# Kernel optimization log

Measured on AMD Instinct MI355X. Metric: run time of the kernel, lower is better.

The kernel has to match this reference:

```python
import jax, jax.numpy as jnp
import numpy as np


def _lstm_layer(x, Wx, Wh, b):
    """Standard LSTM over time. x: [B,T,D], Wx/Wh: [D,4D], b: [4D]. Returns [B,T,D]."""
    B, T, D = x.shape
    # Precompute input contributions for all timesteps (one big GEMM).
    xg = jnp.einsum('btd,dg->btg', x, Wx) + b  # [B,T,4D]

    def step(carry, xg_t):
        h, c = carry
        g = xg_t + h @ Wh  # [B,4D]
        i, f, gg, o = jnp.split(g, 4, axis=-1)
        c = jax.nn.sigmoid(f) * c + jax.nn.sigmoid(i) * jnp.tanh(gg)
        h = jax.nn.sigmoid(o) * jnp.tanh(c)
        return (h, c), h

    h0 = jnp.zeros((B, D), x.dtype)
    c0 = jnp.zeros((B, D), x.dtype)
    (_, _), hs = jax.lax.scan(step, (h0, c0), jnp.swapaxes(xg, 0, 1))  # hs: [T,B,D]
    return jnp.swapaxes(hs, 0, 1)


def setup_inputs() -> dict:
    key = jax.random.key(0)
    ks = jax.random.split(key, 8)
    B, T, V, D = 4, 1024, 32000, 512
    s = 1.0 / np.sqrt(D)
    return {
        'tokens': jax.random.randint(ks[0], (B, T), 0, V, dtype=jnp.int32),
        'embed': jax.random.normal(ks[1], (V, D), jnp.float32),  # stddev=1.0 per embedding_init
        'Wx0': jax.random.normal(ks[2], (D, 4 * D), jnp.float32) * s,
        'Wh0': jax.random.normal(ks[3], (D, 4 * D), jnp.float32) * s,
        'b0': jnp.zeros((4 * D,), jnp.float32),
        'Wx1': jax.random.normal(ks[4], (D, 4 * D), jnp.float32) * s,
        'Wh1': jax.random.normal(ks[5], (D, 4 * D), jnp.float32) * s,
        'b1': jnp.zeros((4 * D,), jnp.float32),
        'Wout': jax.random.normal(ks[6], (D, V), jnp.float32) * s,
        'bout': jnp.zeros((V,), jnp.float32),
    }


def reference(tokens, embed, Wx0, Wh0, b0, Wx1, Wh1, b1, Wout, bout):
    # ShiftRight(axis=1): prepend 0 token, drop last.
    shifted = jnp.pad(tokens, ((0, 0), (1, 0)))[:, :-1]
    x = jnp.take(embed, shifted, axis=0)  # [B,T,D]
    x = _lstm_layer(x, Wx0, Wh0, b0)
    x = _lstm_layer(x, Wx1, Wh1, b1)
    # Dropout is deterministic=True -> identity.
    logits = jnp.einsum('btd,dv->btv', x, Wout) + bout  # [B,T,V]
    return logits
```

## Files before the change

kernel.cpp:

```cpp
#include <hip/hip_runtime.h>
#include <math.h>


#define TSEQ 1024
#define DIM  512
#define GDIM 2048
#define VOC  32000
#define SENT 0x7F7F7F7Fu

typedef unsigned uint4v __attribute__((ext_vector_type(4)));
typedef float    f4v    __attribute__((ext_vector_type(4)));
typedef short    short8 __attribute__((ext_vector_type(8)));
typedef float    f32x4  __attribute__((ext_vector_type(4)));

__device__ __forceinline__ uint4v poll_load16(const unsigned* p) {
    uint4v v;
    asm volatile("global_load_dwordx4 %0, %1, off sc1\n\t"
                 "s_waitcnt vmcnt(0)"
                 : "=v"(v) : "v"(p) : "memory");
    return v;
}

__device__ __forceinline__ float fsig(float x) {
    return __builtin_amdgcn_rcpf(1.0f + __expf(-x));
}
__device__ __forceinline__ float ftanh_(float x) {
    return 1.0f - 2.0f * __builtin_amdgcn_rcpf(1.0f + __expf(2.0f * x));
}

__device__ __forceinline__ unsigned short f2bf(float x) {
    unsigned u = __builtin_bit_cast(unsigned, x);
    return (unsigned short)((u + 0x7FFFu + ((u >> 16) & 1u)) >> 16);
}
__device__ __forceinline__ float bf2f(unsigned short h) {
    return __builtin_bit_cast(float, (unsigned)h << 16);
}

__global__ void embed_kernel(const int* __restrict__ tokens,
                             const float* __restrict__ embed,
                             float* __restrict__ x)
{
    const int row = blockIdx.x;
    const int b = row >> 10;
    const int t = row & 1023;
    const int tok = (t == 0) ? 0 : tokens[b * TSEQ + t - 1];
    const float4* src = (const float4*)(embed + (size_t)tok * DIM);
    float4* dst = (float4*)(x + (size_t)row * DIM);
    dst[threadIdx.x] = src[threadIdx.x];
}

__global__ __launch_bounds__(256) void gemm_bias_f32(
    const float* __restrict__ A, const float* __restrict__ Bm,
    const float* __restrict__ bias, float* __restrict__ C,
    int M, int N, int K)
{
    constexpr int BK = 16;
    __shared__ float As[BK][128 + 4];
    __shared__ float Bs[BK][128 + 4];

    const int tid = threadIdx.x;
    const int m0 = blockIdx.y * 128;
    const int n0 = blockIdx.x * 128;
    const int tm = (tid >> 4) << 3;
    const int tn = (tid & 15) << 3;

    const int a_r = tid >> 2;
    const int a_c = (tid & 3) << 2;
    const int b_r = tid >> 5;
    const int b_c = (tid & 31) << 2;

    float acc[8][8] = {};

    for (int k0 = 0; k0 < K; k0 += BK) {
        const float4 av0 = *(const float4*)&A[(size_t)(m0 + a_r) * K + k0 + a_c];
        const float4 av1 = *(const float4*)&A[(size_t)(m0 + a_r + 64) * K + k0 + a_c];
        const float4 bv0 = *(const float4*)&Bm[(size_t)(k0 + b_r) * N + n0 + b_c];
        const float4 bv1 = *(const float4*)&Bm[(size_t)(k0 + b_r + 8) * N + n0 + b_c];
        __syncthreads();
        As[a_c + 0][a_r] = av0.x;  As[a_c + 1][a_r] = av0.y;
        As[a_c + 2][a_r] = av0.z;  As[a_c + 3][a_r] = av0.w;
        As[a_c + 0][a_r + 64] = av1.x;  As[a_c + 1][a_r + 64] = av1.y;
        As[a_c + 2][a_r + 64] = av1.z;  As[a_c + 3][a_r + 64] = av1.w;
        *(float4*)&Bs[b_r][b_c] = bv0;
        *(float4*)&Bs[b_r + 8][b_c] = bv1;
        __syncthreads();

        #pragma unroll
        for (int kk = 0; kk < BK; ++kk) {
            float a[8], bf[8];
            *(float4*)&a[0]  = *(const float4*)&As[kk][tm];
            *(float4*)&a[4]  = *(const float4*)&As[kk][tm + 4];
            *(float4*)&bf[0] = *(const float4*)&Bs[kk][tn];
            *(float4*)&bf[4] = *(const float4*)&Bs[kk][tn + 4];
            #pragma unroll
            for (int i = 0; i < 8; ++i)
                #pragma unroll
                for (int jx = 0; jx < 8; ++jx)
                    acc[i][jx] += a[i] * bf[jx];
        }
    }

    float bv[8];
    #pragma unroll
    for (int jx = 0; jx < 8; ++jx) bv[jx] = bias[n0 + tn + jx];

    #pragma unroll
    for (int i = 0; i < 8; ++i) {
        float* crow = C + (size_t)(m0 + tm + i) * N + (n0 + tn);
        float4 o0, o1;
        o0.x = acc[i][0] + bv[0]; o0.y = acc[i][1] + bv[1];
        o0.z = acc[i][2] + bv[2]; o0.w = acc[i][3] + bv[3];
        o1.x = acc[i][4] + bv[4]; o1.y = acc[i][5] + bv[5];
        o1.z = acc[i][6] + bv[6]; o1.w = acc[i][7] + bv[7];
        *(float4*)&crow[0] = o0;
        *(float4*)&crow[4] = o1;
    }
}

__global__ __launch_bounds__(512, 1) void lstm2_kernel(
    const float* __restrict__ xg1, const float* __restrict__ Wh0,
    const float* __restrict__ Wx1, const float* __restrict__ Wh1,
    const float* __restrict__ b1,
    float* __restrict__ h1c, float* __restrict__ h2c,
    float* __restrict__ hs2)
{
    const int layer = blockIdx.x >> 6;
    const int wg    = blockIdx.x & 63;
    const int tid   = threadIdx.x;
    const int dbase = wg * 8;
    const int j = tid & 31;
    const int s = tid >> 5;
    const int wcol = (j >> 3) * DIM + dbase + (j & 7);

    __shared__ f4v  hA[DIM];
    __shared__ f4v  hB[DIM];
    __shared__ float part[16][4][32];
    __shared__ float gate_lds[4][32];

    float wr[32], wx[32];
    {
        const float* Wrec = layer ? Wh1 : Wh0;
        #pragma unroll
        for (int r = 0; r < 32; ++r)
            wr[r] = Wrec[(size_t)(s * 32 + r) * GDIM + wcol];
        if (layer) {
            #pragma unroll
            for (int r = 0; r < 32; ++r)
                wx[r] = Wx1[(size_t)(s * 32 + r) * GDIM + wcol];
        }
    }
    float bias2 = 0.f;
    if (layer && tid < 128) bias2 = b1[wcol];

    float c_reg = 0.f;
    const unsigned* h1u = (const unsigned*)h1c;
    const unsigned* h2u = (const unsigned*)h2c;

    if (layer == 0) {
        for (int t = 0; t < TSEQ; ++t) {
            float xgv = 0.f;
            if (tid < 128) xgv = xg1[((size_t)s * TSEQ + t) * GDIM + wcol];

            if (t > 0) {
                const unsigned* p = h1u + ((size_t)(t - 1) * DIM + tid) * 4;
                uint4v u;
                do { u = poll_load16(p); }
                while (u.x == SENT || u.y == SENT || u.z == SENT || u.w == SENT);
                hA[tid] = __builtin_bit_cast(f4v, u);
            } else {
                hA[tid] = f4v{0.f, 0.f, 0.f, 0.f};
            }
            __syncthreads();

            float a0 = 0.f, a1 = 0.f, a2 = 0.f, a3 = 0.f;
            const f4v* hp = &hA[s * 32];
            #pragma unroll
            for (int r = 0; r < 32; ++r) {
                const f4v v = hp[r];
                a0 += v.x * wr[r]; a1 += v.y * wr[r];
                a2 += v.z * wr[r]; a3 += v.w * wr[r];
            }
            part[s][0][j] = a0; part[s][1][j] = a1;
            part[s][2][j] = a2; part[s][3][j] = a3;
            __syncthreads();

            if (tid < 128) {
                float sum = xgv;
                #pragma unroll
                for (int s2 = 0; s2 < 16; ++s2) sum += part[s2][s][j];
                gate_lds[s][j] = sum;
            }
            __syncthreads();

            if (tid < 32) {
                const int ub = tid >> 3, ud = tid & 7;
                const float iv = gate_lds[ub][ 0 + ud];
                const float fv = gate_lds[ub][ 8 + ud];
                const float gv = gate_lds[ub][16 + ud];
                const float ov = gate_lds[ub][24 + ud];
                const float ig = fsig(iv);
                const float fg = fsig(fv);
                const float og = fsig(ov);
                c_reg = fg * c_reg + ig * ftanh_(gv);
                const float hval = og * ftanh_(c_reg);
                __hip_atomic_store(&h1c[((size_t)t * DIM + dbase + ud) * 4 + ub],
                                   hval, __ATOMIC_RELAXED, __HIP_MEMORY_SCOPE_AGENT);
            }
        }
    } else {
        for (int t = 0; t < TSEQ; ++t) {
            if (t > 0) {
                const unsigned* p = h2u + ((size_t)(t - 1) * DIM + tid) * 4;
                uint4v u;
                do { u = poll_load16(p); }
                while (u.x == SENT || u.y == SENT || u.z == SENT || u.w == SENT);
                hB[tid] = __builtin_bit_cast(f4v, u);
            } else {
                hB[tid] = f4v{0.f, 0.f, 0.f, 0.f};
            }
            __syncthreads();

            float a0 = 0.f, a1 = 0.f, a2 = 0.f, a3 = 0.f;
            {
                const f4v* hp = &hB[s * 32];
                #pragma unroll
                for (int r = 0; r < 32; ++r) {
                    const f4v v = hp[r];
                    a0 += v.x * wr[r]; a1 += v.y * wr[r];
                    a2 += v.z * wr[r]; a3 += v.w * wr[r];
                }
            }

            {
                const unsigned* p = h1u + ((size_t)t * DIM + tid) * 4;
                uint4v u;
                do { u = poll_load16(p); }
                while (u.x == SENT || u.y == SENT || u.z == SENT || u.w == SENT);
                hA[tid] = __builtin_bit_cast(f4v, u);
            }
            __syncthreads();
            {
                const f4v* hp = &hA[s * 32];
                #pragma unroll
                for (int r = 0; r < 32; ++r) {
                    const f4v v = hp[r];
                    a0 += v.x * wx[r]; a1 += v.y * wx[r];
                    a2 += v.z * wx[r]; a3 += v.w * wx[r];
                }
            }
            part[s][0][j] = a0; part[s][1][j] = a1;
            part[s][2][j] = a2; part[s][3][j] = a3;
            __syncthreads();

            if (tid < 128) {
                float sum = bias2;
                #pragma unroll
                for (int s2 = 0; s2 < 16; ++s2) sum += part[s2][s][j];
                gate_lds[s][j] = sum;
            }
            __syncthreads();

            if (tid < 32) {
                const int ub = tid >> 3, ud = tid & 7;
                const float iv = gate_lds[ub][ 0 + ud];
                const float fv = gate_lds[ub][ 8 + ud];
                const float gv = gate_lds[ub][16 + ud];
                const float ov = gate_lds[ub][24 + ud];
                const float ig = fsig(iv);
                const float fg = fsig(fv);
                const float og = fsig(ov);
                c_reg = fg * c_reg + ig * ftanh_(gv);
                const float hval = og * ftanh_(c_reg);
                __hip_atomic_store(&h2c[((size_t)t * DIM + dbase + ud) * 4 + ub],
                                   hval, __ATOMIC_RELAXED, __HIP_MEMORY_SCOPE_AGENT);
                hs2[((size_t)ub * TSEQ + t) * DIM + dbase + ud] = hval;
            }
        }
    }
}

__global__ __launch_bounds__(256) void transpose_W(const float* __restrict__ W,
                                                   unsigned short* __restrict__ Wt)
{
    __shared__ float tile[32][256];
    const int tid = threadIdx.x;
    const int n0 = blockIdx.x * 256;
    const int k0 = blockIdx.y * 32;

    #pragma unroll 8
    for (int r = 0; r < 32; ++r)
        tile[r][tid] = W[(size_t)(k0 + r) * VOC + n0 + tid];
    __syncthreads();

    unsigned short pr[64];
    #pragma unroll
    for (int kk = 0; kk < 32; ++kk) {
        const float w = tile[kk][tid];
        const unsigned short h = f2bf(w);
        const unsigned short l = f2bf(w - bf2f(h));
        pr[2 * kk + 0] = h;
        pr[2 * kk + 1] = l;
    }
    unsigned short* dst = Wt + (size_t)(n0 + tid) * 1024 + 2 * k0;
    #pragma unroll
    for (int i = 0; i < 8; ++i)
        *(short8*)(dst + 8 * i) = *(short8*)&pr[8 * i];
}

__global__ __launch_bounds__(64) void convert_A(const float* __restrict__ A,
                                                unsigned short* __restrict__ At)
{
    const int row = blockIdx.x;
    const int tid = threadIdx.x;
    const float4 v0 = *(const float4*)&A[(size_t)row * DIM + tid * 8];
    const float4 v1 = *(const float4*)&A[(size_t)row * DIM + tid * 8 + 4];
    float vals[8] = {v0.x, v0.y, v0.z, v0.w, v1.x, v1.y, v1.z, v1.w};
    unsigned short pr[16];
    #pragma unroll
    for (int i = 0; i < 8; ++i) {
        const unsigned short h = f2bf(vals[i]);
        pr[2 * i + 0] = h;
        pr[2 * i + 1] = h;
    }
    unsigned short* dst = At + (size_t)row * 1024 + tid * 16;
    #pragma unroll
    for (int i = 0; i < 2; ++i)
        *(short8*)(dst + 8 * i) = *(short8*)&pr[8 * i];
}

__global__ __launch_bounds__(256) void mfma_logits(
    const unsigned short* __restrict__ Ab, const unsigned short* __restrict__ Wb,
    const float* __restrict__ bias, float* __restrict__ C)
{
    constexpr int KP = 1024, BK = 64, NKT = KP / BK;
    __shared__ unsigned short As[128 * 64];
    __shared__ unsigned short Bs[128 * 64];

    const int tid  = threadIdx.x;
    const int lane = tid & 63;
    const int w    = tid >> 6;
    const int wm   = w >> 1, wn = w & 1;
    const int m0 = blockIdx.y * 128;
    const int n0 = blockIdx.x * 128;

    const int srow = tid >> 1;
    const int s0   = (tid & 1) * 4;
    const unsigned short* gA = Ab + (size_t)(m0 + srow) * KP + s0 * 8;
    const unsigned short* gB = Wb + (size_t)(n0 + srow) * KP + s0 * 8;
    const int swz = srow & 7;

    f32x4 acc[4][4] = {};
    short8 ra[4], rb[4];

    #pragma unroll
    for (int c = 0; c < 4; ++c) {
        ra[c] = *(const short8*)(gA + c * 8);
        rb[c] = *(const short8*)(gB + c * 8);
    }

    #pragma unroll 1
    for (int kt = 0; kt < NKT; ++kt) {
        __syncthreads();
        #pragma unroll
        for (int c = 0; c < 4; ++c) {
            *(short8*)&As[srow * 64 + ((s0 + c) ^ swz) * 8] = ra[c];
            *(short8*)&Bs[srow * 64 + ((s0 + c) ^ swz) * 8] = rb[c];
        }
        __syncthreads();

        if (kt + 1 < NKT) {
            const int ko = (kt + 1) * BK;
            #pragma unroll
            for (int c = 0; c < 4; ++c) {
                ra[c] = *(const short8*)(gA + ko + c * 8);
                rb[c] = *(const short8*)(gB + ko + c * 8);
            }
        }

        #pragma unroll
        for (int kk = 0; kk < 2; ++kk) {
            const int q = kk * 4 + (lane >> 4);
            short8 a[4], b[4];
            #pragma unroll
            for (int i = 0; i < 4; ++i) {
                const int Ra = wm * 64 + i * 16 + (lane & 15);
                a[i] = *(const short8*)&As[Ra * 64 + (q ^ (Ra & 7)) * 8];
                const int Rb = wn * 64 + i * 16 + (lane & 15);
                b[i] = *(const short8*)&Bs[Rb * 64 + (q ^ (Rb & 7)) * 8];
            }
            #pragma unroll
            for (int i = 0; i < 4; ++i)
                #pragma unroll
                for (int jx = 0; jx < 4; ++jx)
                    acc[i][jx] = __builtin_amdgcn_mfma_f32_16x16x32_bf16(
                        a[i], b[jx], acc[i][jx], 0, 0, 0);
        }
    }

    float bv[4];
    #pragma unroll
    for (int jx = 0; jx < 4; ++jx)
        bv[jx] = bias[n0 + wn * 64 + jx * 16 + (lane & 15)];

    #pragma unroll
    for (int i = 0; i < 4; ++i) {
        #pragma unroll
        for (int jx = 0; jx < 4; ++jx) {
            const int col = n0 + wn * 64 + jx * 16 + (lane & 15);
            #pragma unroll
            for (int r = 0; r < 4; ++r) {
                const int row = m0 + wm * 64 + i * 16 + (lane >> 4) * 4 + r;
                C[(size_t)row * VOC + col] = acc[i][jx][r] + bv[jx];
            }
        }
    }
}

extern "C" void kernel_launch(void* const* d_in, const int* in_sizes, int n_in,
                              void* d_out, int out_size, void* d_ws, size_t ws_size,
                              hipStream_t stream)
{
    const int*   tokens = (const int*)d_in[0];
    const float* embed  = (const float*)d_in[1];
    const float* Wx0    = (const float*)d_in[2];
    const float* Wh0    = (const float*)d_in[3];
    const float* b0     = (const float*)d_in[4];
    const float* Wx1    = (const float*)d_in[5];
    const float* Wh1    = (const float*)d_in[6];
    const float* b1     = (const float*)d_in[7];
    const float* Wout   = (const float*)d_in[8];
    const float* bout   = (const float*)d_in[9];
    float* out = (float*)d_out;

    char* ws = (char*)d_ws;
    float* x   = (float*)(ws);
    float* xg1 = (float*)(ws + ((size_t)8u << 20));
    float* h1c = (float*)(ws + ((size_t)40u << 20));
    float* h2c = (float*)(ws + ((size_t)48u << 20));
    float* hs2 = x;
    unsigned short* At = (unsigned short*)(ws + ((size_t)56u << 20));
    unsigned short* Wt = (unsigned short*)(ws + ((size_t)64u << 20));

    const bool use_mfma = ws_size >= ((size_t)132u << 20);

    hipMemsetAsync(ws + ((size_t)40u << 20), 0x7F, (size_t)16u << 20, stream);

    embed_kernel<<<dim3(4096), dim3(128), 0, stream>>>(tokens, embed, x);
    gemm_bias_f32<<<dim3(16, 32), dim3(256), 0, stream>>>(x, Wx0, b0, xg1, 4096, 2048, 512);

    if (use_mfma)
        transpose_W<<<dim3(125, 16), dim3(256), 0, stream>>>(Wout, Wt);

    lstm2_kernel<<<dim3(128), dim3(512), 0, stream>>>(xg1, Wh0, Wx1, Wh1, b1, h1c, h2c, hs2);

    if (use_mfma) {
        convert_A<<<dim3(4096), dim3(64), 0, stream>>>(hs2, At);
        mfma_logits<<<dim3(250, 32), dim3(256), 0, stream>>>(At, Wt, bout, out);
    } else {
        gemm_bias_f32<<<dim3(250, 32), dim3(256), 0, stream>>>(hs2, Wout, bout, out, 4096, VOC, 512);
    }
}
```

Before: 3.526 ms.

## Fuse LSTM recurrence and logits GEMM into one persistent kernel with progress flags

Merges the two-layer LSTM kernel and the bf16 MFMA logits GEMM into a single launch. Layer-2 blocks write bf16 hidden states directly into the GEMM A buffer and publish a per-block timestep counter. GEMM tiles spin on those counters so the logits for earlier time chunks run while the recurrence is still going, and the separate convert pass is removed. This relies on the recurrence blocks being resident before the GEMM blocks, which is not guaranteed, so the schedule risks deadlock. GEMM tiles may also compete with the latency-bound recurrence for CUs and memory bandwidth.

```diff
diff --git a/kernel.cpp b/kernel.cpp
--- a/kernel.cpp
+++ b/kernel.cpp
@@ -6,6 +6,7 @@
 #define DIM  512
 #define GDIM 2048
 #define VOC  32000
+#define KP   1024
 #define SENT 0x7F7F7F7Fu
 
 typedef unsigned uint4v __attribute__((ext_vector_type(4)));
@@ -16,6 +17,20 @@
 __device__ __forceinline__ uint4v poll_load16(const unsigned* p) {
     uint4v v;
     asm volatile("global_load_dwordx4 %0, %1, off sc1\n\t"
+                 "s_waitcnt vmcnt(0)"
+                 : "=v"(v) : "v"(p) : "memory");
+    return v;
+}
+__device__ __forceinline__ short8 ld16_sc1(const unsigned short* p) {
+    short8 v;
+    asm volatile("global_load_dwordx4 %0, %1, off sc1\n\t"
+                 "s_waitcnt vmcnt(0)"
+                 : "=v"(v) : "v"(p) : "memory");
+    return v;
+}
+__device__ __forceinline__ unsigned ld4_sc1(const unsigned* p) {
+    unsigned v;
+    asm volatile("global_load_dword %0, %1, off sc1\n\t"
                  "s_waitcnt vmcnt(0)"
                  : "=v"(v) : "v"(p) : "memory");
     return v;
@@ -117,168 +132,6 @@
     }
 }
 
-__global__ __launch_bounds__(512, 1) void lstm2_kernel(
-    const float* __restrict__ xg1, const float* __restrict__ Wh0,
-    const float* __restrict__ Wx1, const float* __restrict__ Wh1,
-    const float* __restrict__ b1,
-    float* __restrict__ h1c, float* __restrict__ h2c,
-    float* __restrict__ hs2)
-{
-    const int layer = blockIdx.x >> 6;
-    const int wg    = blockIdx.x & 63;
-    const int tid   = threadIdx.x;
-    const int dbase = wg * 8;
-    const int j = tid & 31;
-    const int s = tid >> 5;
-    const int wcol = (j >> 3) * DIM + dbase + (j & 7);
-
-    __shared__ f4v  hA[DIM];
-    __shared__ f4v  hB[DIM];
-    __shared__ float part[16][4][32];
-    __shared__ float gate_lds[4][32];
-
-    float wr[32], wx[32];
-    {
-        const float* Wrec = layer ? Wh1 : Wh0;
-        #pragma unroll
-        for (int r = 0; r < 32; ++r)
-            wr[r] = Wrec[(size_t)(s * 32 + r) * GDIM + wcol];
-        if (layer) {
-            #pragma unroll
-            for (int r = 0; r < 32; ++r)
-                wx[r] = Wx1[(size_t)(s * 32 + r) * GDIM + wcol];
-        }
-    }
-    float bias2 = 0.f;
-    if (layer && tid < 128) bias2 = b1[wcol];
-
-    float c_reg = 0.f;
-    const unsigned* h1u = (const unsigned*)h1c;
-    const unsigned* h2u = (const unsigned*)h2c;
-
-    if (layer == 0) {
-        for (int t = 0; t < TSEQ; ++t) {
-            float xgv = 0.f;
-            if (tid < 128) xgv = xg1[((size_t)s * TSEQ + t) * GDIM + wcol];
-
-            if (t > 0) {
-                const unsigned* p = h1u + ((size_t)(t - 1) * DIM + tid) * 4;
-                uint4v u;
-                do { u = poll_load16(p); }
-                while (u.x == SENT || u.y == SENT || u.z == SENT || u.w == SENT);
-                hA[tid] = __builtin_bit_cast(f4v, u);
-            } else {
-                hA[tid] = f4v{0.f, 0.f, 0.f, 0.f};
-            }
-            __syncthreads();
-
-            float a0 = 0.f, a1 = 0.f, a2 = 0.f, a3 = 0.f;
-            const f4v* hp = &hA[s * 32];
-            #pragma unroll
-            for (int r = 0; r < 32; ++r) {
-                const f4v v = hp[r];
-                a0 += v.x * wr[r]; a1 += v.y * wr[r];
-                a2 += v.z * wr[r]; a3 += v.w * wr[r];
-            }
-            part[s][0][j] = a0; part[s][1][j] = a1;
-            part[s][2][j] = a2; part[s][3][j] = a3;
-            __syncthreads();
-
-            if (tid < 128) {
-                float sum = xgv;
-                #pragma unroll
-                for (int s2 = 0; s2 < 16; ++s2) sum += part[s2][s][j];
-                gate_lds[s][j] = sum;
-            }
-            __syncthreads();
-
-            if (tid < 32) {
-                const int ub = tid >> 3, ud = tid & 7;
-                const float iv = gate_lds[ub][ 0 + ud];
-                const float fv = gate_lds[ub][ 8 + ud];
-                const float gv = gate_lds[ub][16 + ud];
-                const float ov = gate_lds[ub][24 + ud];
-                const float ig = fsig(iv);
-                const float fg = fsig(fv);
-                const float og = fsig(ov);
-                c_reg = fg * c_reg + ig * ftanh_(gv);
-                const float hval = og * ftanh_(c_reg);
-                __hip_atomic_store(&h1c[((size_t)t * DIM + dbase + ud) * 4 + ub],
-                                   hval, __ATOMIC_RELAXED, __HIP_MEMORY_SCOPE_AGENT);
-            }
-        }
-    } else {
-        for (int t = 0; t < TSEQ; ++t) {
-            if (t > 0) {
-                const unsigned* p = h2u + ((size_t)(t - 1) * DIM + tid) * 4;
-                uint4v u;
-                do { u = poll_load16(p); }
-                while (u.x == SENT || u.y == SENT || u.z == SENT || u.w == SENT);
-                hB[tid] = __builtin_bit_cast(f4v, u);
-            } else {
-                hB[tid] = f4v{0.f, 0.f, 0.f, 0.f};
-            }
-            __syncthreads();
-
-            float a0 = 0.f, a1 = 0.f, a2 = 0.f, a3 = 0.f;
-            {
-                const f4v* hp = &hB[s * 32];
-                #pragma unroll
-                for (int r = 0; r < 32; ++r) {
-                    const f4v v = hp[r];
-                    a0 += v.x * wr[r]; a1 += v.y * wr[r];
-                    a2 += v.z * wr[r]; a3 += v.w * wr[r];
-                }
-            }
-
-            {
-                const unsigned* p = h1u + ((size_t)t * DIM + tid) * 4;
-                uint4v u;
-                do { u = poll_load16(p); }
-                while (u.x == SENT || u.y == SENT || u.z == SENT || u.w == SENT);
-                hA[tid] = __builtin_bit_cast(f4v, u);
-            }
-            __syncthreads();
-            {
-                const f4v* hp = &hA[s * 32];
-                #pragma unroll
-                for (int r = 0; r < 32; ++r) {
-                    const f4v v = hp[r];
-                    a0 += v.x * wx[r]; a1 += v.y * wx[r];
-                    a2 += v.z * wx[r]; a3 += v.w * wx[r];
-                }
-            }
-            part[s][0][j] = a0; part[s][1][j] = a1;
-            part[s][2][j] = a2; part[s][3][j] = a3;
-            __syncthreads();
-
-            if (tid < 128) {
-                float sum = bias2;
-                #pragma unroll
-                for (int s2 = 0; s2 < 16; ++s2) sum += part[s2][s][j];
-                gate_lds[s][j] = sum;
-            }
-            __syncthreads();
-
-            if (tid < 32) {
-                const int ub = tid >> 3, ud = tid & 7;
-                const float iv = gate_lds[ub][ 0 + ud];
-                const float fv = gate_lds[ub][ 8 + ud];
-                const float gv = gate_lds[ub][16 + ud];
-                const float ov = gate_lds[ub][24 + ud];
-                const float ig = fsig(iv);
-                const float fg = fsig(fv);
-                const float og = fsig(ov);
-                c_reg = fg * c_reg + ig * ftanh_(gv);
-                const float hval = og * ftanh_(c_reg);
-                __hip_atomic_store(&h2c[((size_t)t * DIM + dbase + ud) * 4 + ub],
-                                   hval, __ATOMIC_RELAXED, __HIP_MEMORY_SCOPE_AGENT);
-                hs2[((size_t)ub * TSEQ + t) * DIM + dbase + ud] = hval;
-            }
-        }
-    }
-}
-
 __global__ __launch_bounds__(256) void transpose_W(const float* __restrict__ W,
                                                    unsigned short* __restrict__ Wt)
 {
@@ -301,116 +154,289 @@
         pr[2 * kk + 0] = h;
         pr[2 * kk + 1] = l;
     }
-    unsigned short* dst = Wt + (size_t)(n0 + tid) * 1024 + 2 * k0;
+    unsigned short* dst = Wt + (size_t)(n0 + tid) * KP + 2 * k0;
     #pragma unroll
     for (int i = 0; i < 8; ++i)
         *(short8*)(dst + 8 * i) = *(short8*)&pr[8 * i];
 }
 
-__global__ __launch_bounds__(64) void convert_A(const float* __restrict__ A,
-                                                unsigned short* __restrict__ At)
+__global__ __launch_bounds__(512, 1) void mega_kernel(
+    const float* __restrict__ xg1, const float* __restrict__ Wh0,
+    const float* __restrict__ Wx1, const float* __restrict__ Wh1,
+    const float* __restrict__ b1,
+    float* __restrict__ h1c, float* __restrict__ h2c,
+    float* __restrict__ hs2,
+    unsigned* __restrict__ progress,
+    unsigned short* __restrict__ Ab, const unsigned short* __restrict__ Wb,
+    const float* __restrict__ bout, float* __restrict__ out,
+    int use_mfma)
 {
-    const int row = blockIdx.x;
+    __shared__ __align__(16) char smem[86016];
+
     const int tid = threadIdx.x;
-    const float4 v0 = *(const float4*)&A[(size_t)row * DIM + tid * 8];
-    const float4 v1 = *(const float4*)&A[(size_t)row * DIM + tid * 8 + 4];
-    float vals[8] = {v0.x, v0.y, v0.z, v0.w, v1.x, v1.y, v1.z, v1.w};
-    unsigned short pr[16];
-    #pragma unroll
-    for (int i = 0; i < 8; ++i) {
-        const unsigned short h = f2bf(vals[i]);
-        pr[2 * i + 0] = h;
-        pr[2 * i + 1] = h;
-    }
-    unsigned short* dst = At + (size_t)row * 1024 + tid * 16;
-    #pragma unroll
-    for (int i = 0; i < 2; ++i)
-        *(short8*)(dst + 8 * i) = *(short8*)&pr[8 * i];
-}
-
-__global__ __launch_bounds__(256) void mfma_logits(
-    const unsigned short* __restrict__ Ab, const unsigned short* __restrict__ Wb,
-    const float* __restrict__ bias, float* __restrict__ C)
-{
-    constexpr int KP = 1024, BK = 64, NKT = KP / BK;
-    __shared__ unsigned short As[128 * 64];
-    __shared__ unsigned short Bs[128 * 64];
-
-    const int tid  = threadIdx.x;
-    const int lane = tid & 63;
-    const int w    = tid >> 6;
-    const int wm   = w >> 1, wn = w & 1;
-    const int m0 = blockIdx.y * 128;
-    const int n0 = blockIdx.x * 128;
-
-    const int srow = tid >> 1;
-    const int s0   = (tid & 1) * 4;
-    const unsigned short* gA = Ab + (size_t)(m0 + srow) * KP + s0 * 8;
-    const unsigned short* gB = Wb + (size_t)(n0 + srow) * KP + s0 * 8;
-    const int swz = srow & 7;
-
-    f32x4 acc[4][4] = {};
-    short8 ra[4], rb[4];
-
-    #pragma unroll
-    for (int c = 0; c < 4; ++c) {
-        ra[c] = *(const short8*)(gA + c * 8);
-        rb[c] = *(const short8*)(gB + c * 8);
-    }
-
-    #pragma unroll 1
-    for (int kt = 0; kt < NKT; ++kt) {
+
+    if (blockIdx.x < 128) {
+        f4v*   hA       = (f4v*)smem;
+        f4v*   hB       = (f4v*)(smem + 8192);
+        float* partf    = (float*)(smem + 16384);
+        float* gate_lds = (float*)(smem + 24576);
+
+        const int layer = blockIdx.x >> 6;
+        const int wg    = blockIdx.x & 63;
+        const int dbase = wg * 8;
+        const int j = tid & 31;
+        const int s = tid >> 5;
+        const int wcol = (j >> 3) * DIM + dbase + (j & 7);
+
+        float wr[32], wx[32];
+        {
+            const float* Wrec = layer ? Wh1 : Wh0;
+            #pragma unroll
+            for (int r = 0; r < 32; ++r)
+                wr[r] = Wrec[(size_t)(s * 32 + r) * GDIM + wcol];
+            if (layer) {
+                #pragma unroll
+                for (int r = 0; r < 32; ++r)
+                    wx[r] = Wx1[(size_t)(s * 32 + r) * GDIM + wcol];
+            }
+        }
+        float bias2 = 0.f;
+        if (layer && tid < 128) bias2 = b1[wcol];
+
+        float c_reg = 0.f;
+        const unsigned* h1u = (const unsigned*)h1c;
+        const unsigned* h2u = (const unsigned*)h2c;
+        unsigned* Au = (unsigned*)Ab;
+
+        if (layer == 0) {
+            for (int t = 0; t < TSEQ; ++t) {
+                float xgv = 0.f;
+                if (tid < 128) xgv = xg1[((size_t)s * TSEQ + t) * GDIM + wcol];
+
+                if (t > 0) {
+                    const unsigned* p = h1u + ((size_t)(t - 1) * DIM + tid) * 4;
+                    uint4v u;
+                    do { u = poll_load16(p); }
+                    while (u.x == SENT || u.y == SENT || u.z == SENT || u.w == SENT);
+                    hA[tid] = __builtin_bit_cast(f4v, u);
+                } else {
+                    hA[tid] = f4v{0.f, 0.f, 0.f, 0.f};
+                }
+                __syncthreads();
+
+                float a0 = 0.f, a1 = 0.f, a2 = 0.f, a3 = 0.f;
+                const f4v* hp = &hA[s * 32];
+                #pragma unroll
+                for (int r = 0; r < 32; ++r) {
+                    const f4v v = hp[r];
+                    a0 += v.x * wr[r]; a1 += v.y * wr[r];
+                    a2 += v.z * wr[r]; a3 += v.w * wr[r];
+                }
+                partf[(s * 4 + 0) * 32 + j] = a0; partf[(s * 4 + 1) * 32 + j] = a1;
+                partf[(s * 4 + 2) * 32 + j] = a2; partf[(s * 4 + 3) * 32 + j] = a3;
+                __syncthreads();
+
+                if (tid < 128) {
+                    float sum = xgv;
+                    #pragma unroll
+                    for (int s2 = 0; s2 < 16; ++s2) sum += partf[(s2 * 4 + s) * 32 + j];
+                    gate_lds[s * 32 + j] = sum;
+                }
+                __syncthreads();
+
+                if (tid < 32) {
+                    const int ub = tid >> 3, ud = tid & 7;
+                    const float iv = gate_lds[ub * 32 +  0 + ud];
+                    const float fv = gate_lds[ub * 32 +  8 + ud];
+                    const float gv = gate_lds[ub * 32 + 16 + ud];
+                    const float ov = gate_lds[ub * 32 + 24 + ud];
+                    const float ig = fsig(iv);
+                    const float fg = fsig(fv);
+                    const float og = fsig(ov);
+                    c_reg = fg * c_reg + ig * ftanh_(gv);
+                    const float hval = og * ftanh_(c_reg);
+                    __hip_atomic_store(&h1c[((size_t)t * DIM + dbase + ud) * 4 + ub],
+                                       hval, __ATOMIC_RELAXED, __HIP_MEMORY_SCOPE_AGENT);
+                }
+            }
+        } else {
+            for (int t = 0; t < TSEQ; ++t) {
+                if (t > 0) {
+                    const unsigned* p = h2u + ((size_t)(t - 1) * DIM + tid) * 4;
+                    uint4v u;
+                    do { u = poll_load16(p); }
+                    while (u.x == SENT || u.y == SENT || u.z == SENT || u.w == SENT);
+                    hB[tid] = __builtin_bit_cast(f4v, u);
+                } else {
+                    hB[tid] = f4v{0.f, 0.f, 0.f, 0.f};
+                }
+                __syncthreads();
+
+                float a0 = 0.f, a1 = 0.f, a2 = 0.f, a3 = 0.f;
+                {
+                    const f4v* hp = &hB[s * 32];
+                    #pragma unroll
+                    for (int r = 0; r < 32; ++r) {
+                        const f4v v = hp[r];
+                        a0 += v.x * wr[r]; a1 += v.y * wr[r];
+                        a2 += v.z * wr[r]; a3 += v.w * wr[r];
+                    }
+                }
+                {
+                    const unsigned* p = h1u + ((size_t)t * DIM + tid) * 4;
+                    uint4v u;
+                    do { u = poll_load16(p); }
+                    while (u.x == SENT || u.y == SENT || u.z == SENT || u.w == SENT);
+                    hA[tid] = __builtin_bit_cast(f4v, u);
+                }
+                __syncthreads();
+                {
+                    const f4v* hp = &hA[s * 32];
+                    #pragma unroll
+                    for (int r = 0; r < 32; ++r) {
+                        const f4v v = hp[r];
+                        a0 += v.x * wx[r]; a1 += v.y * wx[r];
+                        a2 += v.z * wx[r]; a3 += v.w * wx[r];
+                    }
+                }
+                partf[(s * 4 + 0) * 32 + j] = a0; partf[(s * 4 + 1) * 32 + j] = a1;
+                partf[(s * 4 + 2) * 32 + j] = a2; partf[(s * 4 + 3) * 32 + j] = a3;
+                __syncthreads();
+
+                if (tid < 128) {
+                    float sum = bias2;
+                    #pragma unroll
+                    for (int s2 = 0; s2 < 16; ++s2) sum += partf[(s2 * 4 + s) * 32 + j];
+                    gate_lds[s * 32 + j] = sum;
+                }
+                __syncthreads();
+
+                if (tid < 32) {
+                    const int ub = tid >> 3, ud = tid & 7;
+                    const float iv = gate_lds[ub * 32 +  0 + ud];
+                    const float fv = gate_lds[ub * 32 +  8 + ud];
+                    const float gv = gate_lds[ub * 32 + 16 + ud];
+                    const float ov = gate_lds[ub * 32 + 24 + ud];
+                    const float ig = fsig(iv);
+                    const float fg = fsig(fv);
+                    const float og = fsig(ov);
+                    c_reg = fg * c_reg + ig * ftanh_(gv);
+                    const float hval = og * ftanh_(c_reg);
+                    __hip_atomic_store(&h2c[((size_t)t * DIM + dbase + ud) * 4 + ub],
+                                       hval, __ATOMIC_RELAXED, __HIP_MEMORY_SCOPE_AGENT);
+                    if (use_mfma) {
+                        const unsigned short ah = f2bf(hval);
+                        const unsigned pk = (unsigned)ah | ((unsigned)ah << 16);
+                        __hip_atomic_store(&Au[(size_t)(ub * TSEQ + t) * 512 + dbase + ud],
+                                           pk, __ATOMIC_RELAXED, __HIP_MEMORY_SCOPE_AGENT);
+                    } else {
+                        hs2[((size_t)ub * TSEQ + t) * DIM + dbase + ud] = hval;
+                    }
+                }
+                if (use_mfma) {
+                    if (tid < 64)
+                        asm volatile("s_waitcnt vmcnt(0)" ::: "memory");
+                    if (tid == 0)
+                        __hip_atomic_store(&progress[wg], (unsigned)(t + 1),
+                                           __ATOMIC_RELAXED, __HIP_MEMORY_SCOPE_AGENT);
+                }
+            }
+        }
+    } else {
+        unsigned short* As = (unsigned short*)smem;
+        unsigned short* Bs = (unsigned short*)(smem + 16384);
+
+        const int job = blockIdx.x - 128;
+        const int tw  = job / 1000;
+        const int rem = job % 1000;
+        const int bb  = rem / 250;
+        const int nn  = rem % 250;
+        const int m0  = bb * 1024 + tw * 128;
+        const int n0  = nn * 128;
+
+        const unsigned tneed = (unsigned)(tw * 128 + 128);
+        if (tid < 64) {
+            const unsigned* pp = progress + tid;
+            unsigned v;
+            do { v = ld4_sc1(pp); } while (__any(v < tneed));
+        }
         __syncthreads();
+
+        const int lane = tid & 63;
+        const int w    = tid >> 6;
+        const int wm   = w >> 2;
+        const int wn   = w & 3;
+
+        const int srow = tid >> 2;
+        const int s0   = (tid & 3) * 2;
+        const unsigned short* gA = Ab + (size_t)(m0 + srow) * KP + s0 * 8;
+        const unsigned short* gB = Wb + (size_t)(n0 + srow) * KP + s0 * 8;
+        const int swz = srow & 7;
+
+        f32x4 acc[4][2] = {};
+        short8 ra[2], rb[2];
+
+        ra[0] = ld16_sc1(gA);
+        ra[1] = ld16_sc1(gA + 8);
+        rb[0] = *(const short8*)(gB);
+        rb[1] = *(const short8*)(gB + 8);
+
+        #pragma unroll 1
+        for (int kt = 0; kt < KP / 64; ++kt) {
+            __syncthreads();
+            #pragma unroll
+            for (int c = 0; c < 2; ++c) {
+                *(short8*)&As[srow * 64 + ((s0 + c) ^ swz) * 8] = ra[c];
+                *(short8*)&Bs[srow * 64 + ((s0 + c) ^ swz) * 8] = rb[c];
+            }
+            __syncthreads();
+
+            if (kt + 1 < KP / 64) {
+                const int ko = (kt + 1) * 64;
+                ra[0] = ld16_sc1(gA + ko);
+                ra[1] = ld16_sc1(gA + ko + 8);
+                rb[0] = *(const short8*)(gB + ko);
+                rb[1] = *(const short8*)(gB + ko + 8);
+            }
+
+            #pragma unroll
+            for (int kk = 0; kk < 2; ++kk) {
+                const int q = kk * 4 + (lane >> 4);
+                short8 a[4], b[2];
+                #pragma unroll
+                for (int i = 0; i < 4; ++i) {
+                    const int Ra = wm * 64 + i * 16 + (lane & 15);
+                    a[i] = *(const short8*)&As[Ra * 64 + (q ^ (Ra & 7)) * 8];
+                }
+                #pragma unroll
+                for (int jx = 0; jx < 2; ++jx) {
+                    const int Rb = wn * 32 + jx * 16 + (lane & 15);
+                    b[jx] = *(const short8*)&Bs[Rb * 64 + (q ^ (Rb & 7)) * 8];
+                }
+                #pragma unroll
+                for (int i = 0; i < 4; ++i)
+                    #pragma unroll
+                    for (int jx = 0; jx < 2; ++jx)
+                        acc[i][jx] = __builtin_amdgcn_mfma_f32_16x16x32_bf16(
+                            a[i], b[jx], acc[i][jx], 0, 0, 0);
+            }
+        }
+
+        float bv[2];
         #pragma unroll
-        for (int c = 0; c < 4; ++c) {
-            *(short8*)&As[srow * 64 + ((s0 + c) ^ swz) * 8] = ra[c];
-            *(short8*)&Bs[srow * 64 + ((s0 + c) ^ swz) * 8] = rb[c];
-        }
-        __syncthreads();
-
-        if (kt + 1 < NKT) {
-            const int ko = (kt + 1) * BK;
+        for (int jx = 0; jx < 2; ++jx)
+            bv[jx] = bout[n0 + wn * 32 + jx * 16 + (lane & 15)];
+
+        #pragma unroll
+        for (int i = 0; i < 4; ++i) {
             #pragma unroll
-            for (int c = 0; c < 4; ++c) {
-                ra[c] = *(const short8*)(gA + ko + c * 8);
-                rb[c] = *(const short8*)(gB + ko + c * 8);
-            }
-        }
-
-        #pragma unroll
-        for (int kk = 0; kk < 2; ++kk) {
-            const int q = kk * 4 + (lane >> 4);
-            short8 a[4], b[4];
-            #pragma unroll
-            for (int i = 0; i < 4; ++i) {
-                const int Ra = wm * 64 + i * 16 + (lane & 15);
-                a[i] = *(const short8*)&As[Ra * 64 + (q ^ (Ra & 7)) * 8];
-                const int Rb = wn * 64 + i * 16 + (lane & 15);
-                b[i] = *(const short8*)&Bs[Rb * 64 + (q ^ (Rb & 7)) * 8];
-            }
-            #pragma unroll
-            for (int i = 0; i < 4; ++i)
-                #pragma unroll
-                for (int jx = 0; jx < 4; ++jx)
-                    acc[i][jx] = __builtin_amdgcn_mfma_f32_16x16x32_bf16(
-                        a[i], b[jx], acc[i][jx], 0, 0, 0);
-        }
-    }
-
-    float bv[4];
-    #pragma unroll
-    for (int jx = 0; jx < 4; ++jx)
-        bv[jx] = bias[n0 + wn * 64 + jx * 16 + (lane & 15)];
-
-    #pragma unroll
-    for (int i = 0; i < 4; ++i) {
-        #pragma unroll
-        for (int jx = 0; jx < 4; ++jx) {
-            const int col = n0 + wn * 64 + jx * 16 + (lane & 15);
-            #pragma unroll
-            for (int r = 0; r < 4; ++r) {
-                const int row = m0 + wm * 64 + i * 16 + (lane >> 4) * 4 + r;
-                C[(size_t)row * VOC + col] = acc[i][jx][r] + bv[jx];
+            for (int jx = 0; jx < 2; ++jx) {
+                const int col = n0 + wn * 32 + jx * 16 + (lane & 15);
+                #pragma unroll
+                for (int r = 0; r < 4; ++r) {
+                    const int row = m0 + wm * 64 + i * 16 + (lane >> 4) * 4 + r;
+                    out[(size_t)row * VOC + col] = acc[i][jx][r] + bv[jx];
+                }
             }
         }
     }
@@ -433,30 +459,30 @@
     float* out = (float*)d_out;
 
     char* ws = (char*)d_ws;
-    float* x   = (float*)(ws);
-    float* xg1 = (float*)(ws + ((size_t)8u << 20));
-    float* h1c = (float*)(ws + ((size_t)40u << 20));
-    float* h2c = (float*)(ws + ((size_t)48u << 20));
+    float*    x        = (float*)(ws);
+    float*    xg1      = (float*)(ws + ((size_t)8u << 20));
+    float*    h1c      = (float*)(ws + ((size_t)40u << 20));
+    float*    h2c      = (float*)(ws + ((size_t)48u << 20));
+    unsigned* progress = (unsigned*)(ws + ((size_t)56u << 20));
+    unsigned short* At = (unsigned short*)(ws + ((size_t)57u << 20));
+    unsigned short* Wt = (unsigned short*)(ws + ((size_t)66u << 20));
     float* hs2 = x;
-    unsigned short* At = (unsigned short*)(ws + ((size_t)56u << 20));
-    unsigned short* Wt = (unsigned short*)(ws + ((size_t)64u << 20));
 
     const bool use_mfma = ws_size >= ((size_t)132u << 20);
 
     hipMemsetAsync(ws + ((size_t)40u << 20), 0x7F, (size_t)16u << 20, stream);
+    hipMemsetAsync(progress, 0, 4096, stream);
 
     embed_kernel<<<dim3(4096), dim3(128), 0, stream>>>(tokens, embed, x);
     gemm_bias_f32<<<dim3(16, 32), dim3(256), 0, stream>>>(x, Wx0, b0, xg1, 4096, 2048, 512);
 
-    if (use_mfma)
+    if (use_mfma) {
         transpose_W<<<dim3(125, 16), dim3(256), 0, stream>>>(Wout, Wt);
-
-    lstm2_kernel<<<dim3(128), dim3(512), 0, stream>>>(xg1, Wh0, Wx1, Wh1, b1, h1c, h2c, hs2);
-
-    if (use_mfma) {
-        convert_A<<<dim3(4096), dim3(64), 0, stream>>>(hs2, At);
-        mfma_logits<<<dim3(250, 32), dim3(256), 0, stream>>>(At, Wt, bout, out);
+        mega_kernel<<<dim3(128 + 8000), dim3(512), 0, stream>>>(
+            xg1, Wh0, Wx1, Wh1, b1, h1c, h2c, hs2, progress, At, Wt, bout, out, 1);
     } else {
+        mega_kernel<<<dim3(128), dim3(512), 0, stream>>>(
+            xg1, Wh0, Wx1, Wh1, b1, h1c, h2c, hs2, progress, At, Wt, bout, out, 0);
         gemm_bias_f32<<<dim3(250, 32), dim3(256), 0, stream>>>(hs2, Wout, bout, out, 4096, VOC, 512);
     }
 }
```

New measurement: 4.424 ms. +25.5%, slower.
